# Performance work log

Hardware: AMD Instinct MI355X
Metric: run time of the kernel (lower is better)

Reference implementation:

```python
import jax, jax.numpy as jnp
import numpy as np

# --- configuration constants (match init_kwargs) ---
N = 256          # num_oscillators
T = 200          # simulation steps
INTERVAL = 5     # readout_update_interval
OFFSET = 1       # spike_update_offset
DELAY = 10
D = DELAY + 1    # delay-buffer length
K_GLOBAL = 1.0   # global_coupling_strength
STEP_SIZE = 0.1
GAMMA_ATTR = 0.5 # gamma_attraction_strength
DECAY = 0.9      # membrane_decay
THRESH = 1.0
REC_SCALE = 0.1
ALPHA_FIX = 0.5  # fixed_alpha_value (fixed during training)
CLS_START = 50   # classifier_start_step
SURR_BETA = 4.0  # surrogate-gradient sharpness
NUM_CLASSES = 10


def _spike(u):
    # Heaviside forward, sigmoid surrogate backward (straight-through)
    sg = jax.nn.sigmoid(SURR_BETA * u)
    hard = (u > 0).astype(u.dtype)
    return sg + jax.lax.stop_gradient(hard - sg)


def _forward(x, theta0, W_init, omega, W_ro, W_gate, W_rec, W_fb, W_cls, b_cls):
    B = x.shape[0]
    P = W_gate.shape[1]  # num_pixels = H*W*C
    xf = x.reshape(B, -1)
    gamma0 = jnp.tanh(xf @ W_init)                 # ReadoutLayer.initialize_gamma_from_input -> [B,N]
    buf0 = jnp.tile(theta0[None], (D, 1, 1))       # theta delay buffer [D,B,N]
    zN = jnp.zeros((B, N), x.dtype)
    zP = jnp.zeros((B, P), x.dtype)
    carry0 = (theta0, gamma0, zN, zP, zP, zN, buf0)  # theta, gamma, gate, membrane, spikes, fb-activity a, buffer

    def step(carry, s):
        theta, gamma, gate, mem, spk, a, buf = carry
        # --- KuramotoLayer: dtheta_i = omega_i + K/N * sum_j (1 + W_ij*alpha) sin(th_j - th_i) + attr*gamma_i
        # top-down connectivity W_ij = a_i a_j is rank-1, so the coupling sum is computed exactly in O(N).
        sin_t = jnp.sin(theta); cos_t = jnp.cos(theta)
        S = sin_t.sum(-1, keepdims=True); C = cos_t.sum(-1, keepdims=True)
        base = cos_t * S - sin_t * C
        as_ = jnp.sum(a * sin_t, -1, keepdims=True)
        ac_ = jnp.sum(a * cos_t, -1, keepdims=True)
        weighted = ALPHA_FIX * (cos_t * a * as_ - sin_t * a * ac_)
        dtheta = omega + (K_GLOBAL / N) * (base + weighted) + GAMMA_ATTR * gamma
        theta = theta + STEP_SIZE * dtheta

        # --- ReadoutLayer.gamma_update + SinusoidalGate every INTERVAL steps
        def ro_upd(args):
            g = jnp.tanh(theta @ W_ro)
            gt = g * 0.5 * (1.0 + jnp.cos(theta - buf[0]))  # gate from delayed phase difference
            return g, gt
        gamma, gate = jax.lax.cond((s % INTERVAL) == 0, ro_upd, lambda args: args, (gamma, gate))

        # --- SNNLayer.forward_step + TopDownFeedback on offset spike-update steps
        def sp_upd(args):
            mem_, spk_, a_ = args
            cur = gate @ W_gate + REC_SCALE * (spk_ @ W_rec)
            mem_ = DECAY * mem_ * (1.0 - spk_) + cur       # leaky membrane with reset
            spk_ = _spike(mem_ - THRESH)
            a_ = jnp.tanh(spk_ @ W_fb)                     # per-oscillator feedback activity
            return mem_, spk_, a_
        m_sp = (((s - OFFSET) % INTERVAL) == 0) & (s > OFFSET)
        mem, spk, a = jax.lax.cond(m_sp, sp_upd, lambda args: args, (mem, spk, a))

        buf = jnp.concatenate([buf[1:], theta[None]], axis=0)
        return (theta, gamma, gate, mem, spk, a, buf), spk

    _, spk_hist = jax.lax.scan(step, carry0, jnp.arange(1, T + 1))
    spike_trace = jnp.transpose(spk_hist, (1, 0, 2))       # [B,T,P]
    rate = jnp.mean(spike_trace[:, CLS_START:, :], axis=1) # SNNLayer.classify: mean firing rate
    logits = rate @ W_cls + b_cls
    return logits


def setup_inputs() -> dict:
    key = jax.random.key(0)
    ks = jax.random.split(key, 10)
    B, H, W, C = 32, 32, 32, 3
    P = H * W * C
    x = jax.random.normal(ks[0], (B, H, W, C), jnp.float32)
    theta0 = jax.random.normal(ks[1], (B, N), jnp.float32)
    W_init = jax.random.normal(ks[2], (P, N), jnp.float32) / np.sqrt(P).astype(np.float32)
    omega = jax.random.normal(ks[3], (N,), jnp.float32) * 0.5
    W_ro = jax.random.normal(ks[4], (N, N), jnp.float32) / np.sqrt(N).astype(np.float32)
    W_gate = jax.random.normal(ks[5], (N, P), jnp.float32) / np.sqrt(N).astype(np.float32)
    W_rec = jax.random.normal(ks[6], (P, P), jnp.float32) / np.sqrt(P).astype(np.float32)
    W_fb = jax.random.normal(ks[7], (P, N), jnp.float32) / np.sqrt(P).astype(np.float32)
    W_cls = jax.random.normal(ks[8], (P, NUM_CLASSES), jnp.float32) / np.sqrt(P).astype(np.float32)
    b_cls = jnp.zeros((NUM_CLASSES,), jnp.float32)
    return dict(x=x, theta0=theta0, W_init=W_init, omega=omega, W_ro=W_ro,
                W_gate=W_gate, W_rec=W_rec, W_fb=W_fb, W_cls=W_cls, b_cls=b_cls)


def reference(x, theta0, W_init, omega, W_ro, W_gate, W_rec, W_fb, W_cls, b_cls):
    return _forward(x, theta0, W_init, omega, W_ro, W_gate, W_rec, W_fb, W_cls, b_cls)
```

## Files before the change

kernel.cpp:

```cpp
#include <hip/hip_runtime.h>
#include <cstdint>
#include <cstddef>

#define BB 32
#define NN 256
#define PP 3072
#define NG 192
#define RING 16

typedef unsigned short u16;

__global__ __launch_bounds__(512) void k_init(
    const float* __restrict__ x, const float* __restrict__ W_init,
    double* __restrict__ gpartI, double* __restrict__ memD,
    double* __restrict__ a_g, float* __restrict__ rate,
    u16* __restrict__ maskA, u16* __restrict__ maskB) {
  const int blk = blockIdx.x, tid = threadIdx.x;
  if (blk < 192) {
    const int b = blk / 6, sub = blk % 6;
    __shared__ double xl[512];
    xl[tid] = (double)x[(size_t)b * PP + sub * 512 + tid];
    __syncthreads();
    const int osc = tid & 255, kh = tid >> 8;
    const float* wp = W_init + (size_t)(sub * 512 + kh * 256) * NN + osc;
    const double* xp = xl + kh * 256;
    double a0 = 0, a1 = 0, a2 = 0, a3 = 0, a4 = 0, a5 = 0, a6 = 0, a7 = 0;
    for (int r = 0; r < 256; r += 8) {
      a0 += xp[r + 0] * (double)wp[(size_t)(r + 0) * NN];
      a1 += xp[r + 1] * (double)wp[(size_t)(r + 1) * NN];
      a2 += xp[r + 2] * (double)wp[(size_t)(r + 2) * NN];
      a3 += xp[r + 3] * (double)wp[(size_t)(r + 3) * NN];
      a4 += xp[r + 4] * (double)wp[(size_t)(r + 4) * NN];
      a5 += xp[r + 5] * (double)wp[(size_t)(r + 5) * NN];
      a6 += xp[r + 6] * (double)wp[(size_t)(r + 6) * NN];
      a7 += xp[r + 7] * (double)wp[(size_t)(r + 7) * NN];
    }
    double acc = ((a0 + a1) + (a2 + a3)) + ((a4 + a5) + (a6 + a7));
    __syncthreads();
    __shared__ double hl[256];
    if (kh) hl[osc] = acc;
    __syncthreads();
    if (!kh) gpartI[((size_t)b * 6 + sub) * 256 + osc] = acc + hl[osc];
  } else {
    const int b = blk - 192;
    for (int i = tid; i < PP; i += 512) {
      memD[(size_t)b * PP + i] = 0.0;
      rate[(size_t)b * PP + i] = 0.f;
    }
    for (int i = tid; i < NG; i += 512) {
      maskA[b * NG + i] = 0;
      maskB[b * NG + i] = 0;
    }
    for (int i = tid; i < NN; i += 512) a_g[b * NN + i] = 0.0;
  }
}

__global__ __launch_bounds__(512, 6) void k_rec(
    const float* __restrict__ W_rec, const u16* __restrict__ listG,
    const int* __restrict__ cntG, const int* __restrict__ cnt2G,
    double* __restrict__ recPart, const double* __restrict__ gateG,
    const float* __restrict__ W_gate, double* __restrict__ gatePart) {
  __shared__ double gd[16 * 258];
  __shared__ float wt[256 * 16];
  __shared__ double red[256];
  const int g = blockIdx.x, bh = blockIdx.y, z = blockIdx.z, j0 = g * 16;
  const int tid = threadIdx.x;
  const int pi = tid & 15, bl = (tid >> 4) & 15, h = tid >> 8;
  const int b = bh * 16 + bl, p = j0 + pi, pid = tid & 255;

  if (z < 2) {
    const int mid = cnt2G[b];
    const int beg = z ? mid : 0;
    const int end = z ? cntG[b] : mid;
    const u16* lst = listG + (size_t)b * PP;

    double v0 = 0, v1 = 0, v2 = 0, v3 = 0, v4 = 0, v5 = 0, v6 = 0, v7 = 0;
    int i = beg + h;
    for (; i + 16 <= end; i += 16) {
      const int r0 = lst[i], r1 = lst[i + 2], r2 = lst[i + 4], r3 = lst[i + 6],
                r4 = lst[i + 8], r5 = lst[i + 10], r6 = lst[i + 12],
                r7 = lst[i + 14];
      v0 += (double)W_rec[(size_t)r0 * PP + p];
      v1 += (double)W_rec[(size_t)r1 * PP + p];
      v2 += (double)W_rec[(size_t)r2 * PP + p];
      v3 += (double)W_rec[(size_t)r3 * PP + p];
      v4 += (double)W_rec[(size_t)r4 * PP + p];
      v5 += (double)W_rec[(size_t)r5 * PP + p];
      v6 += (double)W_rec[(size_t)r6 * PP + p];
      v7 += (double)W_rec[(size_t)r7 * PP + p];
    }
    double vr = ((v0 + v1) + (v2 + v3)) + ((v4 + v5) + (v6 + v7));
    for (; i < end; i += 2) vr += (double)W_rec[(size_t)lst[i] * PP + p];

    if (h) red[pid] = vr;
    __syncthreads();
    if (!h) recPart[((size_t)z * BB + b) * PP + p] = vr + red[pid];
  } else {
    for (int i = tid; i < 4096; i += 512) {
      gd[(i >> 8) * 258 + (i & 255)] =
          gateG[(size_t)(bh * 16 + (i >> 8)) * 256 + (i & 255)];
      wt[i] = W_gate[(size_t)(i >> 4) * PP + j0 + (i & 15)];
    }
    __syncthreads();
    double s0 = 0, s1 = 0, s2 = 0, s3 = 0, s4 = 0, s5 = 0, s6 = 0, s7 = 0;
    {
      const double* gq = gd + bl * 258 + h * 128;
      const float* wq = wt + h * 128 * 16 + pi;
      for (int k = 0; k < 128; k += 8) {
        s0 += gq[k + 0] * (double)wq[(k + 0) * 16];
        s1 += gq[k + 1] * (double)wq[(k + 1) * 16];
        s2 += gq[k + 2] * (double)wq[(k + 2) * 16];
        s3 += gq[k + 3] * (double)wq[(k + 3) * 16];
        s4 += gq[k + 4] * (double)wq[(k + 4) * 16];
        s5 += gq[k + 5] * (double)wq[(k + 5) * 16];
        s6 += gq[k + 6] * (double)wq[(k + 6) * 16];
        s7 += gq[k + 7] * (double)wq[(k + 7) * 16];
      }
    }
    double vg = ((s0 + s1) + (s2 + s3)) + ((s4 + s5) + (s6 + s7));
    if (h) red[pid] = vg;
    __syncthreads();
    if (!h) gatePart[(size_t)b * PP + p] = vg + red[pid];
  }
}

__global__ __launch_bounds__(512) void k_fin(
    const u16* __restrict__ mask_rd, u16* __restrict__ mask_wr,
    double* __restrict__ memD, const double* __restrict__ gatePart,
    const double* __restrict__ recPart, float* __restrict__ rate, int accum) {
  const int g = blockIdx.x, tid = threadIdx.x;
  const int pi = tid & 15, b = tid >> 4;
  const int p = g * 16 + pi;
  const size_t idx = (size_t)b * PP + p;
  const double vrs = recPart[idx] + recPart[(size_t)BB * PP + idx];
  const double cur = gatePart[idx] + 0.1 * vrs;
  const double so = (double)((mask_rd[b * NG + g] >> pi) & 1);
  const double mv = 0.9 * memD[idx] * (1.0 - so) + cur;
  const double sv = (mv - 1.0 > 0.0) ? 1.0 : 0.0;
  memD[idx] = mv;
  if (accum) rate[idx] += (float)sv;
  unsigned long long bal = __ballot(sv > 0.5);
  const int lane = tid & 63;
  if ((lane & 15) == 0)
    mask_wr[b * NG + g] = (u16)((bal >> (16 * (lane >> 4))) & 0xFFFFull);
}

__global__ __launch_bounds__(256) void k_fb(
    const u16* __restrict__ spk_mask, u16* __restrict__ listG,
    int* __restrict__ cntG, int* __restrict__ cnt2G,
    const float* __restrict__ W_fb, double* __restrict__ a_part) {
  const int b = blockIdx.x, y = blockIdx.y, tid = threadIdx.x;
  __shared__ int pc[NG], sc[NG];
  __shared__ u16 m_l[NG];
  __shared__ u16 list_l[PP];
  if (tid < NG) {
    m_l[tid] = spk_mask[b * NG + tid];
    pc[tid] = __popc((unsigned int)m_l[tid]);
    sc[tid] = pc[tid];
  }
  __syncthreads();
  for (int d = 1; d < NG; d <<= 1) {
    int v = 0;
    if (tid < NG) v = sc[tid] + ((tid >= d) ? sc[tid - d] : 0);
    __syncthreads();
    if (tid < NG) sc[tid] = v;
    __syncthreads();
  }
  const int total = sc[NG - 1];
  if (tid < NG) {
    int off = sc[tid] - pc[tid];
    unsigned int m = m_l[tid];
    while (m) {
      int bit = __builtin_ctz(m);
      m &= m - 1;
      list_l[off++] = (u16)(tid * 16 + bit);
    }
  }
  __syncthreads();
  if (y == 0) {
    for (int i = tid; i < total; i += 256) listG[(size_t)b * PP + i] = list_l[i];
    if (tid == 0) {
      cntG[b] = total;
      cnt2G[b] = sc[95];
    }
  }
  const int j = tid;
  double c0 = 0, c1 = 0, c2 = 0, c3 = 0, c4 = 0, c5 = 0, c6 = 0, c7 = 0;
  int i = y;
  for (; i + 128 <= total; i += 128) {
    c0 += (double)W_fb[(size_t)list_l[i + 0] * NN + j];
    c1 += (double)W_fb[(size_t)list_l[i + 16] * NN + j];
    c2 += (double)W_fb[(size_t)list_l[i + 32] * NN + j];
    c3 += (double)W_fb[(size_t)list_l[i + 48] * NN + j];
    c4 += (double)W_fb[(size_t)list_l[i + 64] * NN + j];
    c5 += (double)W_fb[(size_t)list_l[i + 80] * NN + j];
    c6 += (double)W_fb[(size_t)list_l[i + 96] * NN + j];
    c7 += (double)W_fb[(size_t)list_l[i + 112] * NN + j];
  }
  double acc = ((c0 + c1) + (c2 + c3)) + ((c4 + c5) + (c6 + c7));
  for (; i < total; i += 16) acc += (double)W_fb[(size_t)list_l[i] * NN + j];
  a_part[((size_t)b * 16 + y) * NN + j] = acc;
}

__global__ __launch_bounds__(512) void k_theta(
    double* __restrict__ ring, double* __restrict__ gamma_g,
    double* __restrict__ a_g, double* __restrict__ gateG,
    const double* __restrict__ a_part, const float* __restrict__ theta0,
    const float* __restrict__ omega, const float* __restrict__ W_ro,
    const double* __restrict__ gpartI, int* __restrict__ cntG,
    int* __restrict__ cnt2G, int k2) {
  const int b = blockIdx.x, tid = threadIdx.x;
  const int j = tid & 255, q = tid >> 8;
  const int lane = tid & 63, wid = tid >> 6;
  __shared__ double th[256];
  __shared__ double red[16];
  __shared__ double qpart[256];

  const int s0 = 5 * k2 + 1, s1 = 5 * k2 + 5;
  double new_a = 0.0;
  if (k2 > 0) {
    double s = 0.0;
#pragma unroll
    for (int u = 0; u < 8; ++u)
      s += a_part[((size_t)b * 16 + q * 8 + u) * NN + j];
    if (q) qpart[j] = s;
    __syncthreads();
    if (!q) new_a = tanh(s + qpart[j]);
    __syncthreads();
  }

  double t = 0.0, aj = 0.0, gm = 0.0, om = 0.0;
  if (!q) {
    om = (double)omega[j];
    if (k2 == 0) {
      double s = 0.0;
      for (int c6 = 0; c6 < 6; ++c6) s += gpartI[((size_t)b * 6 + c6) * 256 + j];
      gm = tanh(s);
      t = (double)theta0[b * NN + j];
      ring[0 * BB * NN + b * NN + j] = t;
      if (tid == 0) {
        cntG[b] = 0;
        cnt2G[b] = 0;
      }
    } else {
      t = ring[((s0 - 1) & (RING - 1)) * BB * NN + b * NN + j];
      aj = a_g[b * NN + j];
      gm = gamma_g[b * NN + j];
    }
  }

  for (int s = s0; s <= s1; ++s) {
    if (!q && k2 > 0 && s == s0 + 1) {
      aj = new_a;
      a_g[b * NN + j] = aj;
    }
    double sn = 0.0, cs = 0.0;
    if (!q) sincos(t, &sn, &cs);
    double r0 = sn, r1 = cs, r2 = aj * sn, r3 = aj * cs;
#pragma unroll
    for (int o = 32; o; o >>= 1) {
      r0 += __shfl_down(r0, o);
      r1 += __shfl_down(r1, o);
      r2 += __shfl_down(r2, o);
      r3 += __shfl_down(r3, o);
    }
    if (lane == 0 && wid < 4) {
      red[wid * 4 + 0] = r0;
      red[wid * 4 + 1] = r1;
      red[wid * 4 + 2] = r2;
      red[wid * 4 + 3] = r3;
    }
    __syncthreads();
    double S = red[0] + red[4] + red[8] + red[12];
    double C = red[1] + red[5] + red[9] + red[13];
    double AS = red[2] + red[6] + red[10] + red[14];
    double AC = red[3] + red[7] + red[11] + red[15];
    __syncthreads();
    if (!q) {
      double base = cs * S - sn * C;
      double wgt = 0.5 * (cs * aj * AS - sn * aj * AC);
      t = t + 0.1 * (om + (1.0 / 256.0) * (base + wgt) + 0.5 * gm);
      ring[(s & (RING - 1)) * BB * NN + b * NN + j] = t;
    }
  }
  if (!q) th[j] = t;
  __syncthreads();
  {
    double c0 = 0, c1 = 0, c2 = 0, c3 = 0, c4 = 0, c5 = 0, c6 = 0, c7 = 0;
    const float* wp = W_ro + j;
    const int i0 = q * 128;
    for (int i = 0; i < 128; i += 8) {
      c0 += th[i0 + i + 0] * (double)wp[(size_t)(i0 + i + 0) * NN];
      c1 += th[i0 + i + 1] * (double)wp[(size_t)(i0 + i + 1) * NN];
      c2 += th[i0 + i + 2] * (double)wp[(size_t)(i0 + i + 2) * NN];
      c3 += th[i0 + i + 3] * (double)wp[(size_t)(i0 + i + 3) * NN];
      c4 += th[i0 + i + 4] * (double)wp[(size_t)(i0 + i + 4) * NN];
      c5 += th[i0 + i + 5] * (double)wp[(size_t)(i0 + i + 5) * NN];
      c6 += th[i0 + i + 6] * (double)wp[(size_t)(i0 + i + 6) * NN];
      c7 += th[i0 + i + 7] * (double)wp[(size_t)(i0 + i + 7) * NN];
    }
    double acc = ((c0 + c1) + (c2 + c3)) + ((c4 + c5) + (c6 + c7));
    if (q) qpart[j] = acc;
    __syncthreads();
    if (!q) {
      double gnew = tanh(acc + qpart[j]);
      gamma_g[b * NN + j] = gnew;
      int sd = s1 - 11;
      if (sd < 0) sd = 0;
      double dly = ring[(sd & (RING - 1)) * BB * NN + b * NN + j];
      double gt = gnew * 0.5 * (1.0 + cos(t - dly));
      gateG[(size_t)b * 256 + j] = gt;
    }
  }
}

__global__ __launch_bounds__(256) void k_cls(const float* __restrict__ rate,
                                             const float* __restrict__ Wcls,
                                             const float* __restrict__ bcls,
                                             float* __restrict__ out) {
  const int b = blockIdx.x, t = threadIdx.x;
  double acc[10];
#pragma unroll
  for (int c = 0; c < 10; ++c) acc[c] = 0.0;
  for (int p = t; p < PP; p += 256) {
    double r = (double)rate[(size_t)b * PP + p] / 30.0;
#pragma unroll
    for (int c = 0; c < 10; ++c) acc[c] += r * (double)Wcls[(size_t)p * 10 + c];
  }
  __shared__ double sh[10][256];
#pragma unroll
  for (int c = 0; c < 10; ++c) sh[c][t] = acc[c];
  __syncthreads();
  for (int off = 128; off; off >>= 1) {
    if (t < off)
#pragma unroll
      for (int c = 0; c < 10; ++c) sh[c][t] += sh[c][t + off];
    __syncthreads();
  }
  if (t < 10) out[b * 10 + t] = (float)(sh[t][0] + (double)bcls[t]);
}

extern "C" void kernel_launch(void* const* d_in, const int* in_sizes, int n_in,
                              void* d_out, int out_size, void* d_ws,
                              size_t ws_size, hipStream_t stream) {
  const float* x = (const float*)d_in[0];
  const float* theta0 = (const float*)d_in[1];
  const float* W_init = (const float*)d_in[2];
  const float* omega = (const float*)d_in[3];
  const float* W_ro = (const float*)d_in[4];
  const float* W_gate = (const float*)d_in[5];
  const float* W_rec = (const float*)d_in[6];
  const float* W_fb = (const float*)d_in[7];
  const float* W_cls = (const float*)d_in[8];
  const float* b_cls = (const float*)d_in[9];

  char* w = (char*)d_ws;
  size_t off = 0;
  auto alloc = [&](size_t sz) -> void* {
    void* p = w + off;
    off = (off + sz + 255) & ~(size_t)255;
    return p;
  };
  double* ring = (double*)alloc((size_t)RING * BB * NN * 8);
  double* gamma = (double*)alloc((size_t)BB * NN * 8);
  double* a_g = (double*)alloc((size_t)BB * NN * 8);
  double* gateG = (double*)alloc((size_t)BB * NN * 8);
  double* memD = (double*)alloc((size_t)BB * PP * 8);
  float* rate = (float*)alloc((size_t)BB * PP * 4);
  u16* maskA = (u16*)alloc((size_t)BB * NG * 2);
  u16* maskB = (u16*)alloc((size_t)BB * NG * 2);
  u16* listG = (u16*)alloc((size_t)BB * PP * 2);
  int* cntG = (int*)alloc((size_t)BB * 4);
  int* cnt2G = (int*)alloc((size_t)BB * 4);
  double* gpartI = (double*)alloc((size_t)BB * 6 * 256 * 8);
  double* a_part = (double*)alloc((size_t)BB * 16 * NN * 8);
  double* recPart = (double*)alloc((size_t)2 * BB * PP * 8);
  double* gatePart = (double*)alloc((size_t)BB * PP * 8);

  k_init<<<224, 512, 0, stream>>>(x, W_init, gpartI, memD, a_g, rate, maskA,
                                  maskB);
  k_theta<<<32, 512, 0, stream>>>(ring, gamma, a_g, gateG, a_part, theta0,
                                  omega, W_ro, gpartI, cntG, cnt2G, 0);
  for (int k = 1; k < 40; ++k) {
    const u16* mrd = (k & 1) ? maskA : maskB;
    u16* mwr = (k & 1) ? maskB : maskA;
    k_rec<<<dim3(192, 2, 3), 512, 0, stream>>>(W_rec, listG, cntG, cnt2G,
                                               recPart, gateG, W_gate,
                                               gatePart);
    k_fin<<<192, 512, 0, stream>>>(mrd, mwr, memD, gatePart, recPart, rate,
                                   (k >= 10) ? 1 : 0);
    k_fb<<<dim3(32, 16), 256, 0, stream>>>(mwr, listG, cntG, cnt2G, W_fb,
                                           a_part);
    k_theta<<<32, 512, 0, stream>>>(ring, gamma, a_g, gateG, a_part, theta0,
                                    omega, W_ro, gpartI, cntG, cnt2G, k);
  }
  k_cls<<<32, 256, 0, stream>>>(rate, W_cls, b_cls, (float*)d_out);
}
```

Before: 2.288 ms.

## Fuse membrane update into feedback kernel with redundant per-block recompute

Merges the k_fin membrane/spike update into the feedback kernel. Each of the 16 y-blocks per batch recomputes the full membrane update and builds the spike mask in shared memory, so the separate mask round-trip through global memory goes away. Membrane state is double-buffered so redundant readers never see partially written data, and only y==0 writes state and rate. This removes one kernel launch per step (39 in total) but makes each feedback block read the recurrent, gate and membrane arrays redundantly, multiplying global traffic by 16.

```diff
diff --git a/kernel.cpp b/kernel.cpp
--- a/kernel.cpp
+++ b/kernel.cpp
@@ -124,37 +124,41 @@
   }
 }
 
-__global__ __launch_bounds__(512) void k_fin(
-    const u16* __restrict__ mask_rd, u16* __restrict__ mask_wr,
-    double* __restrict__ memD, const double* __restrict__ gatePart,
-    const double* __restrict__ recPart, float* __restrict__ rate, int accum) {
-  const int g = blockIdx.x, tid = threadIdx.x;
-  const int pi = tid & 15, b = tid >> 4;
-  const int p = g * 16 + pi;
-  const size_t idx = (size_t)b * PP + p;
-  const double vrs = recPart[idx] + recPart[(size_t)BB * PP + idx];
-  const double cur = gatePart[idx] + 0.1 * vrs;
-  const double so = (double)((mask_rd[b * NG + g] >> pi) & 1);
-  const double mv = 0.9 * memD[idx] * (1.0 - so) + cur;
-  const double sv = (mv - 1.0 > 0.0) ? 1.0 : 0.0;
-  memD[idx] = mv;
-  if (accum) rate[idx] += (float)sv;
-  unsigned long long bal = __ballot(sv > 0.5);
-  const int lane = tid & 63;
-  if ((lane & 15) == 0)
-    mask_wr[b * NG + g] = (u16)((bal >> (16 * (lane >> 4))) & 0xFFFFull);
-}
-
-__global__ __launch_bounds__(256) void k_fb(
-    const u16* __restrict__ spk_mask, u16* __restrict__ listG,
+__global__ __launch_bounds__(256) void k_fb2(
+    const u16* __restrict__ maskOld, u16* __restrict__ maskNew,
+    const double* __restrict__ memOld, double* __restrict__ memNew,
+    const double* __restrict__ gatePart, const double* __restrict__ recPart,
+    float* __restrict__ rate, int accum, u16* __restrict__ listG,
     int* __restrict__ cntG, int* __restrict__ cnt2G,
     const float* __restrict__ W_fb, double* __restrict__ a_part) {
   const int b = blockIdx.x, y = blockIdx.y, tid = threadIdx.x;
   __shared__ int pc[NG], sc[NG];
   __shared__ u16 m_l[NG];
   __shared__ u16 list_l[PP];
+
+  const int lane = tid & 63;
+  for (int c = 0; c < 12; ++c) {
+    const int p = c * 256 + tid;
+    const int g = p >> 4;
+    const size_t idx = (size_t)b * PP + p;
+    const double vrs = recPart[idx] + recPart[(size_t)BB * PP + idx];
+    const double cur = gatePart[idx] + 0.1 * vrs;
+    const double so = (double)((maskOld[b * NG + g] >> (p & 15)) & 1);
+    const double mv = 0.9 * memOld[idx] * (1.0 - so) + cur;
+    const double sv = (mv - 1.0 > 0.0) ? 1.0 : 0.0;
+    if (y == 0) {
+      memNew[idx] = mv;
+      if (accum) rate[idx] += (float)sv;
+    }
+    unsigned long long bal = __ballot(sv > 0.5);
+    if ((lane & 15) == 0)
+      m_l[g] = (u16)((bal >> (16 * (lane >> 4))) & 0xFFFFull);
+  }
+  __syncthreads();
+  if (y == 0)
+    for (int i = tid; i < NG; i += 256) maskNew[b * NG + i] = m_l[i];
+
   if (tid < NG) {
-    m_l[tid] = spk_mask[b * NG + tid];
     pc[tid] = __popc((unsigned int)m_l[tid]);
     sc[tid] = pc[tid];
   }
@@ -365,7 +369,8 @@
   double* gamma = (double*)alloc((size_t)BB * NN * 8);
   double* a_g = (double*)alloc((size_t)BB * NN * 8);
   double* gateG = (double*)alloc((size_t)BB * NN * 8);
-  double* memD = (double*)alloc((size_t)BB * PP * 8);
+  double* memA = (double*)alloc((size_t)BB * PP * 8);
+  double* memB = (double*)alloc((size_t)BB * PP * 8);
   float* rate = (float*)alloc((size_t)BB * PP * 4);
   u16* maskA = (u16*)alloc((size_t)BB * NG * 2);
   u16* maskB = (u16*)alloc((size_t)BB * NG * 2);
@@ -377,20 +382,21 @@
   double* recPart = (double*)alloc((size_t)2 * BB * PP * 8);
   double* gatePart = (double*)alloc((size_t)BB * PP * 8);
 
-  k_init<<<224, 512, 0, stream>>>(x, W_init, gpartI, memD, a_g, rate, maskA,
+  k_init<<<224, 512, 0, stream>>>(x, W_init, gpartI, memA, a_g, rate, maskA,
                                   maskB);
   k_theta<<<32, 512, 0, stream>>>(ring, gamma, a_g, gateG, a_part, theta0,
                                   omega, W_ro, gpartI, cntG, cnt2G, 0);
   for (int k = 1; k < 40; ++k) {
     const u16* mrd = (k & 1) ? maskA : maskB;
     u16* mwr = (k & 1) ? maskB : maskA;
+    const double* mOld = (k & 1) ? memA : memB;
+    double* mNew = (k & 1) ? memB : memA;
     k_rec<<<dim3(192, 2, 3), 512, 0, stream>>>(W_rec, listG, cntG, cnt2G,
                                                recPart, gateG, W_gate,
                                                gatePart);
-    k_fin<<<192, 512, 0, stream>>>(mrd, mwr, memD, gatePart, recPart, rate,
-                                   (k >= 10) ? 1 : 0);
-    k_fb<<<dim3(32, 16), 256, 0, stream>>>(mwr, listG, cntG, cnt2G, W_fb,
-                                           a_part);
+    k_fb2<<<dim3(32, 16), 256, 0, stream>>>(mrd, mwr, mOld, mNew, gatePart,
+                                            recPart, rate, (k >= 10) ? 1 : 0,
+                                            listG, cntG, cnt2G, W_fb, a_part);
     k_theta<<<32, 512, 0, stream>>>(ring, gamma, a_g, gateG, a_part, theta0,
                                     omega, W_ro, gpartI, cntG, cnt2G, k);
   }
```

New measurement: 2.418 ms. +5.7%, slower.
